# Kernel tuning notes

Measured on AMD Instinct MI355X. Metric: run time of the kernel, lower is better.

## Reference

```python
import jax, jax.numpy as jnp
import numpy as np

B, N, D_IN, H, D_OUT = 64, 512, 1024, 1024, 1024
EPS = 1e-5          # torch BatchNorm1d default eps
NEG_SLOPE = 0.01    # torch leaky_relu default


def setup_inputs() -> dict:
    key = jax.random.key(0)
    ks = jax.random.split(key, 12)
    s_in = 1.0 / np.sqrt(D_IN)
    s_h = 1.0 / np.sqrt(H)
    return {
        "x": jax.random.normal(ks[0], (B, N, D_IN), dtype=jnp.float32),
        # weights stored as [in, out] so y = x @ W + b
        "W1": jax.random.uniform(ks[1], (D_IN, H), jnp.float32, -s_in, s_in),
        "b1": jax.random.uniform(ks[2], (H,), jnp.float32, -s_in, s_in),
        "gamma": jnp.ones((N,), jnp.float32),
        "beta": jnp.zeros((N,), jnp.float32),
        "W2": jax.random.uniform(ks[3], (D_IN, H), jnp.float32, -s_in, s_in),
        "b2": jax.random.uniform(ks[4], (H,), jnp.float32, -s_in, s_in),
        "W3": jax.random.uniform(ks[5], (H, D_OUT), jnp.float32, -s_h, s_h),
        "b3": jax.random.uniform(ks[6], (D_OUT,), jnp.float32, -s_h, s_h),
        "W4": jax.random.uniform(ks[7], (D_IN, D_OUT), jnp.float32, -s_in, s_in),
        "b4": jax.random.uniform(ks[8], (D_OUT,), jnp.float32, -s_in, s_in),
    }


def reference(x, W1, b1, gamma, beta, W2, b2, W3, b3, W4, b4):
    h = W1.shape[1]
    # theta_x = leaky_relu(bn(l1(x)))
    t = x @ W1 + b1                                   # [B, N, H]
    # BatchNorm1d(num_input): channel dim is N; train-mode batch stats over (B, H)
    mean = jnp.mean(t, axis=(0, 2), keepdims=True)
    var = jnp.var(t, axis=(0, 2), keepdims=True)      # biased variance (torch norm path)
    t = gamma[None, :, None] * (t - mean) * jax.lax.rsqrt(var + EPS) + beta[None, :, None]
    t = jnp.where(t >= 0, t, NEG_SLOPE * t)
    # sigma = theta @ M @ theta^T with M = (I - 1/h)/h  ==  mean-center rows then scale by 1/h
    tM = (t - jnp.mean(t, axis=-1, keepdims=True)) / h  # [B, N, H]
    sigma = jnp.einsum("bnh,bmh->bnm", tM, t)           # [B, N, N]
    att = sigma / jnp.sqrt(jnp.float32(h))              # normal_factor = sqrt(hidden)
    # GLOBAL softmax over the full flattened N*N matrix per batch element
    bsz, n = x.shape[0], x.shape[1]
    att = jax.nn.softmax(att.reshape(bsz, -1), axis=1).reshape(bsz, n, n)
    g = x @ W2 + b2                                     # [B, N, H]
    p = jnp.einsum("bnm,bmh->bnh", att, g) @ W3 + b3    # [B, N, D_OUT]
    phi = x @ W4 + b4                                   # [B, N, D_OUT]
    return phi + p
```

## Files before the change

### kernel.cpp

```cpp
#include <hip/hip_runtime.h>
#include <hip/hip_bf16.h>

typedef _Float16 f16x8 __attribute__((ext_vector_type(8)));
typedef _Float16 f16x4 __attribute__((ext_vector_type(4)));
typedef float    f32x4 __attribute__((ext_vector_type(4)));

#define EPS_ 1e-5f

__device__ __forceinline__ void gload_lds16(const _Float16* g, _Float16* l) {
    __builtin_amdgcn_global_load_lds(
        (const __attribute__((address_space(1))) void*)g,
        (__attribute__((address_space(3))) void*)l, 16, 0, 0);
}


__global__ void k_cvt_f16(const float* __restrict__ in, _Float16* __restrict__ out, int n4) {
    int i = blockIdx.x * blockDim.x + threadIdx.x;
    int stride = gridDim.x * blockDim.x;
    const float4* in4 = (const float4*)in;
    for (; i < n4; i += stride) {
        float4 v = in4[i];
        f16x4 o;
        o[0] = (_Float16)v.x; o[1] = (_Float16)v.y;
        o[2] = (_Float16)v.z; o[3] = (_Float16)v.w;
        *(f16x4*)(out + (size_t)i * 4) = o;
    }
}

__global__ void k_transpose_w(const float* __restrict__ in, _Float16* __restrict__ out) {
    __shared__ float tile[32][33];
    int bx = blockIdx.x * 32;
    int by = blockIdx.y * 32;
    int tx = threadIdx.x, ty = threadIdx.y;
    #pragma unroll
    for (int r = 0; r < 32; r += 8)
        tile[ty + r][tx] = in[(size_t)(by + ty + r) * 1024 + bx + tx];
    __syncthreads();
    #pragma unroll
    for (int r = 0; r < 32; r += 8)
        out[(size_t)(bx + ty + r) * 1024 + by + tx] = (_Float16)tile[tx][ty + r];
}

__global__ void k_b23(const float* __restrict__ b2, const float* __restrict__ W3,
                      float* __restrict__ b23) {
    const int oo = threadIdx.x & 63, hc = threadIdx.x >> 6;
    const int o = blockIdx.x * 64 + oo;
    float s = 0.f;
    for (int h = hc * 256; h < hc * 256 + 256; ++h) s += b2[h] * W3[(size_t)h * 1024 + o];
    __shared__ float red[4][64];
    red[hc][oo] = s;
    __syncthreads();
    if (threadIdx.x < 64) {
        int o2 = blockIdx.x * 64 + threadIdx.x;
        b23[o2] = red[0][threadIdx.x] + red[1][threadIdx.x] + red[2][threadIdx.x] + red[3][threadIdx.x];
    }
}


__global__ void k_bnstats(const _Float16* __restrict__ t, const float* __restrict__ gamma,
                          const float* __restrict__ beta, float* __restrict__ scale,
                          float* __restrict__ shift) {
    const int n = blockIdx.x, tid = threadIdx.x;
    float s = 0.f, s2 = 0.f;
    const _Float16* base = t + (size_t)n * 1024 + tid * 4;
    for (int b = 0; b < 64; ++b) {
        f16x4 v = *(const f16x4*)(base + (size_t)b * 512 * 1024);
        float x0 = (float)v[0], x1 = (float)v[1], x2 = (float)v[2], x3 = (float)v[3];
        s  += x0 + x1 + x2 + x3;
        s2 += x0 * x0 + x1 * x1 + x2 * x2 + x3 * x3;
    }
    #pragma unroll
    for (int o = 32; o > 0; o >>= 1) { s += __shfl_down(s, o); s2 += __shfl_down(s2, o); }
    __shared__ float rs_[4], rs2_[4];
    int lane = tid & 63, w = tid >> 6;
    if (lane == 0) { rs_[w] = s; rs2_[w] = s2; }
    __syncthreads();
    if (tid == 0) {
        float S  = rs_[0] + rs_[1] + rs_[2] + rs_[3];
        float S2 = rs2_[0] + rs2_[1] + rs2_[2] + rs2_[3];
        float mean = S * (1.f / 65536.f);
        float var  = S2 * (1.f / 65536.f) - mean * mean;
        float r = rsqrtf(var + EPS_);
        float sc = gamma[n] * r;
        scale[n] = sc;
        shift[n] = beta[n] - mean * sc;
    }
}

__global__ void k_bnorm(const _Float16* __restrict__ t, const float* __restrict__ scale,
                        const float* __restrict__ shift, _Float16* __restrict__ theta,
                        float* __restrict__ mu) {
    const int row = blockIdx.x, tid = threadIdx.x;
    const int n = row & 511;
    const float sc = scale[n], sh = shift[n];
    f16x4 v = *(const f16x4*)(t + (size_t)row * 1024 + tid * 4);
    float a0 = fmaf((float)v[0], sc, sh); a0 = a0 >= 0.f ? a0 : 0.01f * a0;
    float a1 = fmaf((float)v[1], sc, sh); a1 = a1 >= 0.f ? a1 : 0.01f * a1;
    float a2 = fmaf((float)v[2], sc, sh); a2 = a2 >= 0.f ? a2 : 0.01f * a2;
    float a3 = fmaf((float)v[3], sc, sh); a3 = a3 >= 0.f ? a3 : 0.01f * a3;
    float s = a0 + a1 + a2 + a3;
    #pragma unroll
    for (int o = 32; o > 0; o >>= 1) s += __shfl_down(s, o);
    __shared__ float red[4];
    int lane = tid & 63, w = tid >> 6;
    if (lane == 0) red[w] = s;
    __syncthreads();
    const float mean = (red[0] + red[1] + red[2] + red[3]) * (1.f / 1024.f);
    f16x4 th;
    th[0] = (_Float16)a0; th[1] = (_Float16)a1; th[2] = (_Float16)a2; th[3] = (_Float16)a3;
    *(f16x4*)(theta + (size_t)row * 1024 + tid * 4) = th;
    if (tid == 0) mu[row] = mean;
}

__global__ void k_ssum(const float* __restrict__ part, float* __restrict__ rsum,
                       float* __restrict__ ssum) {
    const int b = blockIdx.x, j = threadIdx.x;
    const int idx = b * 512 + j;
    float s = part[idx] + part[32768 + idx] + part[65536 + idx] + part[98304 + idx];
    rsum[idx] = s;
    #pragma unroll
    for (int o = 32; o > 0; o >>= 1) s += __shfl_down(s, o);
    __shared__ float red[8];
    if ((j & 63) == 0) red[j >> 6] = s;
    __syncthreads();
    if (j == 0) {
        float tt = 0.f;
        #pragma unroll
        for (int k = 0; k < 8; k++) tt += red[k];
        ssum[b] = tt;
    }
}


template <int MODE>
__global__ __launch_bounds__(256) void k_gemm(
    const _Float16* __restrict__ A0, const _Float16* __restrict__ B0,
    const float* __restrict__ auxA, float* __restrict__ auxW,
    void* __restrict__ outp) {

    constexpr int BK = 32;
    __shared__ _Float16 Al[4096];
    __shared__ _Float16 Bl[4096];

    const int tid = threadIdx.x, lane = tid & 63, w = tid >> 6;
    const int wm = w >> 1, wn = w & 1;

    int bm, bn, bz;
    if constexpr (MODE == 1) {
        const int p = blockIdx.x;
        if (p < 4)      { bm = 0; bn = p; }
        else if (p < 7) { bm = 1; bn = p - 3; }
        else if (p < 9) { bm = 2; bn = p - 5; }
        else            { bm = 3; bn = 3; }
        bz = blockIdx.z;
    } else {
        bm = blockIdx.x; bn = blockIdx.y; bz = blockIdx.z;
    }

    const int srow = tid >> 2;
    const int skofs = ((tid & 3) ^ ((tid >> 3) & 3)) * 8;
    _Float16* lA0 = &Al[(w * 64) * 8];
    _Float16* lA1 = &Al[(256 + w * 64) * 8];
    _Float16* lB0 = &Bl[(w * 64) * 8];
    _Float16* lB1 = &Bl[(256 + w * 64) * 8];

    const int lr = lane & 15, kg = lane >> 4;
    const int kswz = kg ^ ((lr >> 1) & 3);

    f32x4 acc[4][4] = {};

    const size_t aO = ((size_t)bz * 512 + bm * 128) * 1024;
    const size_t bO = ((size_t)bz * 512 + bn * 128) * 1024;
    for (int k0 = 0; k0 < 1024; k0 += BK) {
        gload_lds16(A0 + aO + (size_t)srow * 1024 + k0 + skofs, lA0);
        gload_lds16(A0 + aO + (size_t)(srow + 64) * 1024 + k0 + skofs, lA1);
        gload_lds16(B0 + bO + (size_t)srow * 1024 + k0 + skofs, lB0);
        gload_lds16(B0 + bO + (size_t)(srow + 64) * 1024 + k0 + skofs, lB1);
        __syncthreads();
        f16x8 af[4], bf[4];
        #pragma unroll
        for (int m = 0; m < 4; m++)
            af[m] = *(const f16x8*)&Al[((wm * 64 + m * 16 + lr) * 4 + kswz) * 8];
        #pragma unroll
        for (int n = 0; n < 4; n++)
            bf[n] = *(const f16x8*)&Bl[((wn * 64 + n * 16 + lr) * 4 + kswz) * 8];
        #pragma unroll
        for (int m = 0; m < 4; m++)
            #pragma unroll
            for (int n = 0; n < 4; n++)
                acc[m][n] = __builtin_amdgcn_mfma_f32_16x16x32_f16(af[m], bf[n], acc[m][n], 0, 0, 0);
        __syncthreads();
    }

    if constexpr (MODE == 1) {
        __shared__ float rbuf[2][128];
        __shared__ float cbuf[2][128];
        __shared__ _Float16 T[128][136];
        const bool diag = (bm == bn);
        _Float16* o = (_Float16*)outp + (size_t)bz * 262144;
        float csn[4] = {0.f, 0.f, 0.f, 0.f};
        #pragma unroll
        for (int m = 0; m < 4; m++) {
            const int r0 = wm * 64 + m * 16 + kg * 4;
            float rs[4] = {0.f, 0.f, 0.f, 0.f};
            #pragma unroll
            for (int n = 0; n < 4; n++) {
                const int cl = wn * 64 + n * 16 + lr;
                const int gc = bn * 128 + cl;
                const float mj = auxA[bz * 512 + gc];
                f16x4 pk;
                #pragma unroll
                for (int i = 0; i < 4; i++) {
                    const float mi = auxA[bz * 512 + bm * 128 + r0 + i];
                    const float e = __expf(acc[m][n][i] * (1.f / 32768.f) - mi * mj * (1.f / 32.f));
                    o[(size_t)(bm * 128 + r0 + i) * 512 + gc] = (_Float16)e;
                    pk[i] = (_Float16)e;
                    rs[i] += e;
                    csn[n] += e;
                }
                if (!diag) *(f16x4*)&T[cl][r0] = pk;
            }
            #pragma unroll
            for (int i = 0; i < 4; i++) {
                float v = rs[i];
                v += __shfl_xor(v, 1); v += __shfl_xor(v, 2);
                v += __shfl_xor(v, 4); v += __shfl_xor(v, 8);
                if (lr == 0) rbuf[wn][r0 + i] = v;
            }
        }
        if (!diag) {
            #pragma unroll
            for (int n = 0; n < 4; n++) {
                float v = csn[n];
                v += __shfl_xor(v, 16); v += __shfl_xor(v, 32);
                if (kg == 0) cbuf[wm][wn * 64 + n * 16 + lr] = v;
            }
        }
        __syncthreads();
        if (tid < 128) {
            auxW[(size_t)bn * 32768 + bz * 512 + bm * 128 + tid] = rbuf[0][tid] + rbuf[1][tid];
            if (!diag)
                auxW[(size_t)bm * 32768 + bz * 512 + bn * 128 + tid] = cbuf[0][tid] + cbuf[1][tid];
        }
        if (!diag) {
            #pragma unroll
            for (int k = 0; k < 8; k++) {
                const int q = k * 256 + tid;
                const int c = q >> 4, j = q & 15;
                f16x8 v = *(const f16x8*)&T[c][j * 8];
                *(f16x8*)(o + (size_t)(bn * 128 + c) * 512 + bm * 128 + j * 8) = v;
            }
        }
    } else {
        _Float16* o = (_Float16*)outp;
        #pragma unroll
        for (int m = 0; m < 4; m++) {
            #pragma unroll
            for (int n = 0; n < 4; n++) {
                const int r0 = wm * 64 + m * 16 + kg * 4;
                const int gc = bn * 128 + wn * 64 + n * 16 + lr;
                #pragma unroll
                for (int i = 0; i < 4; i++)
                    o[(size_t)(bm * 128 + r0 + i) * 1024 + gc] = (_Float16)acc[m][n][i];
            }
        }
    }
}


template <int MODE>
__global__ __launch_bounds__(512) void k_gemm8(
    const _Float16* __restrict__ A0, const _Float16* __restrict__ B0,
    const _Float16* __restrict__ A1, const _Float16* __restrict__ B1,
    const float* __restrict__ biasf, const float* __restrict__ biasg,
    const float* __restrict__ auxA, const float* __restrict__ auxB,
    const float* __restrict__ sumptr, void* __restrict__ outp) {

    __shared__ _Float16 LA[32768];
    __shared__ _Float16 LB[32768];

    const int tid = threadIdx.x, lane = tid & 63, wid = tid >> 6;
    const int wm = wid >> 2, wn = wid & 3;
    const int lr = lane & 15, kq = lane >> 4;

    int bm, bn, bz = 0;
    if constexpr (MODE == 6) {
        const int swz = (blockIdx.x & 7) * 128 + (blockIdx.x >> 3);
        bm = swz >> 3; bn = swz & 7;
    } else {
        const int swz = (blockIdx.x & 7) * 64 + (blockIdx.x >> 3);
        if constexpr (MODE == 3) { bz = swz >> 3; bm = (swz >> 2) & 1; bn = swz & 3; }
        else { bm = swz >> 2; bn = swz & 3; }
    }

    constexpr int NITER = (MODE == 3) ? 12 : 8;
    float oscale = 1.f;
    if constexpr (MODE == 3) oscale = 1.f / sumptr[bz];

    const int i0 = tid >> 3;
    const int kgs = (tid & 7) ^ (i0 & 7);

    auto STAGE = [&](int g, int isA, int h) {
        const _Float16* P; int ld; size_t off; int kk;
        if constexpr (MODE == 3) {
            if (g < 8) {
                kk = g * 64;
                if (isA) { P = A0; ld = 512;  off = (size_t)bz * 262144 + (size_t)bm * 256 * 512; }
                else     { P = B0; ld = 512;  off = (size_t)bz * 524288 + (size_t)bn * 256 * 512; }
            } else {
                kk = (g - 8) * 64;
                if (isA) { P = A1; ld = 1024; off = ((size_t)bz * 512 + bm * 256) * 1024; }
                else     { P = B1; ld = 1024; off = (size_t)bn * 256 * 1024; }
            }
        } else {
            kk = g * 64;
            if (isA) { P = A0; ld = 1024; off = (size_t)bm * 256 * 1024; }
            else     { P = B0; ld = 1024; off = (size_t)bn * 256 * 1024; }
        }
        const int l0 = isA ? (h * 64 + i0)
                           : ((i0 >> 5) * 64 + h * 32 + (i0 & 31));
        const int l1 = isA ? (128 + h * 64 + i0)
                           : (((i0 >> 5) + 2) * 64 + h * 32 + (i0 & 31));
        _Float16* dst = (isA ? LA : LB) + ((g & 1) * 2 + h) * 8192 + wid * 512;
        gload_lds16(P + off + (size_t)l0 * ld + kk + kgs * 8, dst);
        gload_lds16(P + off + (size_t)l1 * ld + kk + kgs * 8, dst + 4096);
    };

    f32x4 acc[8][4] = {};

    STAGE(0, 1, 0); STAGE(0, 0, 0); STAGE(0, 0, 1); STAGE(0, 1, 1);
    STAGE(1, 0, 0); STAGE(1, 0, 1); STAGE(1, 1, 0);
    asm volatile("s_waitcnt vmcnt(6)" ::: "memory");
    __builtin_amdgcn_s_barrier();

    for (int i = 0; i < NITER; ++i) {
        if constexpr (MODE == 3) {
            if (i == 4) {
                #pragma unroll
                for (int m = 0; m < 8; m++)
                    #pragma unroll
                    for (int n = 0; n < 4; n++)
                        #pragma unroll
                        for (int v = 0; v < 4; v++) acc[m][n][v] *= oscale;
            }
        }
        const bool more = (i + 1 < NITER);
        #pragma unroll
        for (int kt = 0; kt < 2; ++kt) {
            f16x8 bf[4][2];
            #pragma unroll
            for (int sub = 0; sub < 4; ++sub) {
                const int ph = kt * 4 + sub;
                if (sub == 0) {
                    #pragma unroll
                    for (int n = 0; n < 4; n++) {
                        const _Float16* Bs = LB + (kt * 2 + (n >> 1)) * 8192;
                        #pragma unroll
                        for (int s = 0; s < 2; s++)
                            bf[n][s] = *(const f16x8*)&Bs[(wn * 32 + (n & 1) * 16 + lr) * 64
                                                           + ((((s << 2) | kq) ^ (lr & 7)) << 3)];
                    }
                }
                const _Float16* As = LA + (kt * 2 + (sub >> 1)) * 8192;
                f16x8 af[2][2];
                #pragma unroll
                for (int j = 0; j < 2; j++) {
                    const int m = sub * 2 + j;
                    #pragma unroll
                    for (int s = 0; s < 2; s++)
                        af[j][s] = *(const f16x8*)&As[(wm * 64 + (m & 3) * 16 + lr) * 64
                                                       + ((((s << 2) | kq) ^ (lr & 7)) << 3)];
                }
                {
                    constexpr int gof[8] = {1, 2, 2, 2, 2, 3, 3, 3};
                    constexpr int isa[8] = {1, 0, 0, 1, 1, 0, 0, 1};
                    constexpr int hh [8] = {1, 0, 1, 0, 1, 0, 1, 0};
                    if (ph == 0 || more) STAGE(2 * i + gof[ph], isa[ph], hh[ph]);
                }
                __builtin_amdgcn_s_barrier();
                asm volatile("s_waitcnt lgkmcnt(0)" ::: "memory");
                __builtin_amdgcn_sched_barrier(0);
                __builtin_amdgcn_s_setprio(1);
                #pragma unroll
                for (int j = 0; j < 2; j++)
                    #pragma unroll
                    for (int n = 0; n < 4; n++)
                        #pragma unroll
                        for (int s = 0; s < 2; s++)
                            acc[sub * 2 + j][n] = __builtin_amdgcn_mfma_f32_16x16x32_f16(
                                af[j][s], bf[n][s], acc[sub * 2 + j][n], 0, 0, 0);
                __builtin_amdgcn_s_setprio(0);
                if (ph == 1) { if (more) asm volatile("s_waitcnt vmcnt(10)" ::: "memory");
                               else      asm volatile("s_waitcnt vmcnt(8)"  ::: "memory"); }
                if (ph == 3) { if (more) asm volatile("s_waitcnt vmcnt(8)"  ::: "memory");
                               else      asm volatile("s_waitcnt vmcnt(2)"  ::: "memory"); }
                if (ph == 5) { if (more) asm volatile("s_waitcnt vmcnt(10)" ::: "memory");
                               else      asm volatile("s_waitcnt vmcnt(0)"  ::: "memory"); }
                if (ph == 7) { if (more) asm volatile("s_waitcnt vmcnt(8)"  ::: "memory"); }
                __builtin_amdgcn_s_barrier();
            }
        }
    }

    #pragma unroll
    for (int m = 0; m < 8; m++) {
        #pragma unroll
        for (int n = 0; n < 4; n++) {
            const int gc = bn * 256 + wn * 64 + n * 16 + lr;
            const int gr0 = bm * 256 + wm * 128 + m * 16 + kq * 4;
            if constexpr (MODE == 6) {
                if (gc < 1024) {
                    _Float16* o = (_Float16*)outp;
                    const float bias = biasf[gc];
                    #pragma unroll
                    for (int i = 0; i < 4; i++)
                        o[(size_t)(gr0 + i) * 1024 + gc] = (_Float16)(acc[m][n][i] + bias);
                } else {
                    _Float16* o = (_Float16*)B1;
                    const int oc = gc - 1024;
                    const int bb = gr0 >> 9, mm = gr0 & 511;
                    f16x4 pk;
                    #pragma unroll
                    for (int i = 0; i < 4; i++) pk[i] = (_Float16)acc[m][n][i];
                    *(f16x4*)(o + ((size_t)bb * 1024 + oc) * 512 + mm) = pk;
                }
            } else {
                float* o = (float*)outp;
                const float tail = biasf[gc] + biasg[gc];
                const float b23v = auxB[gc];
                #pragma unroll
                for (int i = 0; i < 4; i++) {
                    const int row = gr0 + i;
                    o[((size_t)bz * 512 + row) * 1024 + gc] =
                        acc[m][n][i] + auxA[bz * 512 + row] * oscale * b23v + tail;
                }
            }
        }
    }
}


extern "C" void kernel_launch(void* const* d_in, const int* in_sizes, int n_in,
                              void* d_out, int out_size, void* d_ws, size_t ws_size,
                              hipStream_t stream) {
    (void)in_sizes; (void)n_in; (void)out_size; (void)ws_size;
    const float* x     = (const float*)d_in[0];
    const float* W1    = (const float*)d_in[1];
    const float* b1    = (const float*)d_in[2];
    const float* gamma = (const float*)d_in[3];
    const float* beta  = (const float*)d_in[4];
    const float* W2    = (const float*)d_in[5];
    const float* b2    = (const float*)d_in[6];
    const float* W3    = (const float*)d_in[7];
    const float* b3    = (const float*)d_in[8];
    const float* W4    = (const float*)d_in[9];
    const float* b4    = (const float*)d_in[10];

    char* wsb = (char*)d_ws;
    const size_t MB = 1024 * 1024;
    _Float16* xb    = (_Float16*)(wsb);
    _Float16* Wcat  = (_Float16*)(wsb + 64 * MB);
    _Float16* W1t   = Wcat;
    _Float16* W23t  = Wcat + 1024 * 1024;
    _Float16* W3t   = (_Float16*)(wsb + 68 * MB);
    _Float16* W4t   = (_Float16*)(wsb + 70 * MB);
    _Float16* W2h   = (_Float16*)(wsb + 72 * MB);
    float*    b23   = (float*)(wsb + 74 * MB);
    float*    scl   = (float*)(wsb + 74 * MB + 8192);
    float*    shf   = (float*)(wsb + 74 * MB + 16384);
    float*    ssum  = (float*)(wsb + 74 * MB + 24576);
    float*    mu    = (float*)(wsb + 75 * MB);
    float*    rsum  = (float*)(wsb + 76 * MB);
    float*    rpart = (float*)(wsb + 77 * MB);
    _Float16* t     = (_Float16*)(wsb + 80 * MB);
    _Float16* theta = (_Float16*)(wsb + 144 * MB);
    _Float16* att   = (_Float16*)(wsb + 208 * MB);
    _Float16* gwt   = (_Float16*)(wsb + 240 * MB);

    k_cvt_f16<<<8192, 256, 0, stream>>>(x, xb, 64 * 512 * 1024 / 4);
    k_cvt_f16<<<1024, 256, 0, stream>>>(W2, W2h, 1024 * 1024 / 4);
    dim3 tb(32, 8), tg(32, 32);
    k_transpose_w<<<tg, tb, 0, stream>>>(W1, W1t);
    k_transpose_w<<<tg, tb, 0, stream>>>(W3, W3t);
    k_transpose_w<<<tg, tb, 0, stream>>>(W4, W4t);
    k_gemm<5><<<dim3(8, 8, 1), 256, 0, stream>>>(W3t, W2h, nullptr, nullptr, W23t);
    k_b23<<<16, 256, 0, stream>>>(b2, W3, b23);
    k_gemm8<6><<<1024, 512, 0, stream>>>(xb, Wcat, nullptr, gwt,
        b1, nullptr, nullptr, nullptr, nullptr, t);
    k_bnstats<<<512, 256, 0, stream>>>(t, gamma, beta, scl, shf);
    k_bnorm<<<32768, 256, 0, stream>>>(t, scl, shf, theta, mu);
    k_gemm<1><<<dim3(10, 1, 64), 256, 0, stream>>>(theta, theta, mu, rpart, att);
    k_ssum<<<64, 512, 0, stream>>>(rpart, rsum, ssum);
    k_gemm8<3><<<512, 512, 0, stream>>>(att, gwt, xb, W4t,
        b3, b4, rsum, b23, ssum, d_out);
}
```

Baseline: 449.2 us.

## Fuse BatchNorm sum/sumsq into GEMM epilogue and merge weight transposes

The first GEMM epilogue now computes per-row partial sums and sums of squares of the biased output using shuffles and shared-memory reduction, writing them to a small partial buffer. The BN stats kernel then reads only these partials instead of re-reading the whole 64MB fp16 activation tensor. The three weight transposes are merged into one launch, and the x conversion grid is reduced. This adds epilogue work and extra barriers to the GEMM, and statistics now come from fp32 values before the fp16 rounding.

```diff
diff --git a/kernel.cpp b/kernel.cpp
--- a/kernel.cpp
+++ b/kernel.cpp
@@ -27,7 +27,11 @@
     }
 }
 
-__global__ void k_transpose_w(const float* __restrict__ in, _Float16* __restrict__ out) {
+__global__ void k_transpose_w3(const float* __restrict__ Wa, const float* __restrict__ Wb,
+                               const float* __restrict__ Wc, _Float16* __restrict__ oa,
+                               _Float16* __restrict__ ob, _Float16* __restrict__ oc) {
+    const float* in = blockIdx.z == 0 ? Wa : (blockIdx.z == 1 ? Wb : Wc);
+    _Float16* out   = blockIdx.z == 0 ? oa : (blockIdx.z == 1 ? ob : oc);
     __shared__ float tile[32][33];
     int bx = blockIdx.x * 32;
     int by = blockIdx.y * 32;
@@ -57,29 +61,25 @@
 }
 
 
-__global__ void k_bnstats(const _Float16* __restrict__ t, const float* __restrict__ gamma,
-                          const float* __restrict__ beta, float* __restrict__ scale,
-                          float* __restrict__ shift) {
+__global__ void k_bnstats2(const float* __restrict__ spart, const float* __restrict__ gamma,
+                           const float* __restrict__ beta, float* __restrict__ scale,
+                           float* __restrict__ shift) {
     const int n = blockIdx.x, tid = threadIdx.x;
-    float s = 0.f, s2 = 0.f;
-    const _Float16* base = t + (size_t)n * 1024 + tid * 4;
-    for (int b = 0; b < 64; ++b) {
-        f16x4 v = *(const f16x4*)(base + (size_t)b * 512 * 1024);
-        float x0 = (float)v[0], x1 = (float)v[1], x2 = (float)v[2], x3 = (float)v[3];
-        s  += x0 + x1 + x2 + x3;
-        s2 += x0 * x0 + x1 * x1 + x2 * x2 + x3 * x3;
-    }
+    const int b = tid >> 2, c = tid & 3;
+    const int row = b * 512 + n;
+    float s = spart[c * 32768 + row];
+    float q = spart[131072 + c * 32768 + row];
     #pragma unroll
-    for (int o = 32; o > 0; o >>= 1) { s += __shfl_down(s, o); s2 += __shfl_down(s2, o); }
-    __shared__ float rs_[4], rs2_[4];
+    for (int o = 32; o > 0; o >>= 1) { s += __shfl_down(s, o); q += __shfl_down(q, o); }
+    __shared__ float rs_[4], rq_[4];
     int lane = tid & 63, w = tid >> 6;
-    if (lane == 0) { rs_[w] = s; rs2_[w] = s2; }
+    if (lane == 0) { rs_[w] = s; rq_[w] = q; }
     __syncthreads();
     if (tid == 0) {
-        float S  = rs_[0] + rs_[1] + rs_[2] + rs_[3];
-        float S2 = rs2_[0] + rs2_[1] + rs2_[2] + rs2_[3];
+        float S = rs_[0] + rs_[1] + rs_[2] + rs_[3];
+        float Q = rq_[0] + rq_[1] + rq_[2] + rq_[3];
         float mean = S * (1.f / 65536.f);
-        float var  = S2 * (1.f / 65536.f) - mean * mean;
+        float var  = Q * (1.f / 65536.f) - mean * mean;
         float r = rsqrtf(var + EPS_);
         float sc = gamma[n] * r;
         scale[n] = sc;
@@ -402,21 +402,58 @@
         }
     }
 
-    #pragma unroll
-    for (int m = 0; m < 8; m++) {
-        #pragma unroll
-        for (int n = 0; n < 4; n++) {
-            const int gc = bn * 256 + wn * 64 + n * 16 + lr;
-            const int gr0 = bm * 256 + wm * 128 + m * 16 + kq * 4;
-            if constexpr (MODE == 6) {
-                if (gc < 1024) {
-                    _Float16* o = (_Float16*)outp;
+    if constexpr (MODE == 6) {
+        if (bn < 4) {
+            _Float16* o = (_Float16*)outp;
+            float* sbuf = (float*)LA;
+            float* qbuf = (float*)LB;
+            __syncthreads();
+            #pragma unroll
+            for (int m = 0; m < 8; m++) {
+                float s4[4] = {0.f, 0.f, 0.f, 0.f}, q4[4] = {0.f, 0.f, 0.f, 0.f};
+                const int gr0 = bm * 256 + wm * 128 + m * 16 + kq * 4;
+                #pragma unroll
+                for (int n = 0; n < 4; n++) {
+                    const int gc = bn * 256 + wn * 64 + n * 16 + lr;
                     const float bias = biasf[gc];
                     #pragma unroll
-                    for (int i = 0; i < 4; i++)
-                        o[(size_t)(gr0 + i) * 1024 + gc] = (_Float16)(acc[m][n][i] + bias);
-                } else {
-                    _Float16* o = (_Float16*)B1;
+                    for (int i = 0; i < 4; i++) {
+                        const float e = acc[m][n][i] + bias;
+                        o[(size_t)(gr0 + i) * 1024 + gc] = (_Float16)e;
+                        s4[i] += e; q4[i] += e * e;
+                    }
+                }
+                #pragma unroll
+                for (int i = 0; i < 4; i++) {
+                    float s = s4[i], q = q4[i];
+                    s += __shfl_xor(s, 1); q += __shfl_xor(q, 1);
+                    s += __shfl_xor(s, 2); q += __shfl_xor(q, 2);
+                    s += __shfl_xor(s, 4); q += __shfl_xor(q, 4);
+                    s += __shfl_xor(s, 8); q += __shfl_xor(q, 8);
+                    if (lr == 0) {
+                        const int rl = wm * 128 + m * 16 + kq * 4 + i;
+                        sbuf[wn * 256 + rl] = s;
+                        qbuf[wn * 256 + rl] = q;
+                    }
+                }
+            }
+            __syncthreads();
+            if (tid < 256) {
+                const float s = sbuf[tid] + sbuf[256 + tid] + sbuf[512 + tid] + sbuf[768 + tid];
+                const float q = qbuf[tid] + qbuf[256 + tid] + qbuf[512 + tid] + qbuf[768 + tid];
+                float* sp = (float*)auxB;
+                const int row = bm * 256 + tid;
+                sp[bn * 32768 + row] = s;
+                sp[131072 + bn * 32768 + row] = q;
+            }
+        } else {
+            _Float16* o = (_Float16*)B1;
+            #pragma unroll
+            for (int m = 0; m < 8; m++) {
+                #pragma unroll
+                for (int n = 0; n < 4; n++) {
+                    const int gc = bn * 256 + wn * 64 + n * 16 + lr;
+                    const int gr0 = bm * 256 + wm * 128 + m * 16 + kq * 4;
                     const int oc = gc - 1024;
                     const int bb = gr0 >> 9, mm = gr0 & 511;
                     f16x4 pk;
@@ -424,7 +461,15 @@
                     for (int i = 0; i < 4; i++) pk[i] = (_Float16)acc[m][n][i];
                     *(f16x4*)(o + ((size_t)bb * 1024 + oc) * 512 + mm) = pk;
                 }
-            } else {
+            }
+        }
+    } else {
+        #pragma unroll
+        for (int m = 0; m < 8; m++) {
+            #pragma unroll
+            for (int n = 0; n < 4; n++) {
+                const int gc = bn * 256 + wn * 64 + n * 16 + lr;
+                const int gr0 = bm * 256 + wm * 128 + m * 16 + kq * 4;
                 float* o = (float*)outp;
                 const float tail = biasf[gc] + biasg[gc];
                 const float b23v = auxB[gc];
@@ -472,22 +517,21 @@
     float*    mu    = (float*)(wsb + 75 * MB);
     float*    rsum  = (float*)(wsb + 76 * MB);
     float*    rpart = (float*)(wsb + 77 * MB);
+    float*    spart = (float*)(wsb + 78 * MB);
     _Float16* t     = (_Float16*)(wsb + 80 * MB);
     _Float16* theta = (_Float16*)(wsb + 144 * MB);
     _Float16* att   = (_Float16*)(wsb + 208 * MB);
     _Float16* gwt   = (_Float16*)(wsb + 240 * MB);
 
-    k_cvt_f16<<<8192, 256, 0, stream>>>(x, xb, 64 * 512 * 1024 / 4);
+    k_cvt_f16<<<2048, 256, 0, stream>>>(x, xb, 64 * 512 * 1024 / 4);
     k_cvt_f16<<<1024, 256, 0, stream>>>(W2, W2h, 1024 * 1024 / 4);
-    dim3 tb(32, 8), tg(32, 32);
-    k_transpose_w<<<tg, tb, 0, stream>>>(W1, W1t);
-    k_transpose_w<<<tg, tb, 0, stream>>>(W3, W3t);
-    k_transpose_w<<<tg, tb, 0, stream>>>(W4, W4t);
+    dim3 tb(32, 8), tg3(32, 32, 3);
+    k_transpose_w3<<<tg3, tb, 0, stream>>>(W1, W3, W4, W1t, W3t, W4t);
     k_gemm<5><<<dim3(8, 8, 1), 256, 0, stream>>>(W3t, W2h, nullptr, nullptr, W23t);
     k_b23<<<16, 256, 0, stream>>>(b2, W3, b23);
     k_gemm8<6><<<1024, 512, 0, stream>>>(xb, Wcat, nullptr, gwt,
-        b1, nullptr, nullptr, nullptr, nullptr, t);
-    k_bnstats<<<512, 256, 0, stream>>>(t, gamma, beta, scl, shf);
+        b1, nullptr, nullptr, spart, nullptr, t);
+    k_bnstats2<<<512, 256, 0, stream>>>(spart, gamma, beta, scl, shf);
     k_bnorm<<<32768, 256, 0, stream>>>(t, scl, shf, theta, mu);
     k_gemm<1><<<dim3(10, 1, 64), 256, 0, stream>>>(theta, theta, mu, rpart, att);
     k_ssum<<<64, 512, 0, stream>>>(rpart, rsum, ssum);
```

Result: faster. 436.8 us (-2.7%).
